# Kernel optimization log

Measured on AMD Instinct MI355X. Metric: run time of the kernel, lower is better.

Reference implementation:

```python
import jax, jax.numpy as jnp
import numpy as np

B, T, I, H = 64, 512, 1024, 1024


def setup_inputs() -> dict:
    key = jax.random.key(0)
    k1, k2, k3, k4 = jax.random.split(key, 4)
    scale_ih = (6.0 / (H + I)) ** 0.5  # xavier_uniform bound
    scale_hh = (6.0 / (H + H)) ** 0.5
    return {
        "x": jax.random.normal(k1, (B, T, I), dtype=jnp.float32),
        "h0": jax.random.normal(k2, (1, B, H), dtype=jnp.float32),
        "W_ih": jax.random.uniform(k3, (H, I), dtype=jnp.float32, minval=-scale_ih, maxval=scale_ih),
        "b_ih": jnp.zeros((H,), dtype=jnp.float32),
        "W_hh": jax.random.uniform(k4, (H, H), dtype=jnp.float32, minval=-scale_hh, maxval=scale_hh),
        "b_hh": jnp.zeros((H,), dtype=jnp.float32),
    }


def reference(x, h0, W_ih, b_ih, W_hh, b_hh):
    # h_t = tanh(x_t @ W_ih^T + b_ih + h_{t-1} @ W_hh^T + b_hh)
    # Precompute the input projection for all timesteps (same math, batched GEMM).
    xp = jnp.einsum("bti,hi->tbh", x, W_ih) + b_ih  # [T,B,H]
    h = h0[0]  # [B,H]

    def step(h, xp_t):
        h_new = jnp.tanh(xp_t + h @ W_hh.T + b_hh)
        return h_new, h_new

    _, ys = jax.lax.scan(step, h, xp)  # ys: [T,B,H]
    return jnp.transpose(ys, (1, 0, 2))  # [B,T,H]
```

## Files before the change

kernel.cpp:

```cpp
#include <hip/hip_runtime.h>
#include <hip/hip_bf16.h>

#define BB_   64
#define TT_   512
#define II_   1024
#define HH_   1024

typedef _Float16 half8  __attribute__((ext_vector_type(8)));
typedef _Float16 half4v __attribute__((ext_vector_type(4)));
typedef float    f32x4  __attribute__((ext_vector_type(4)));

__global__ __launch_bounds__(256) void gemm_xp(const float* __restrict__ x,
                                               const float* __restrict__ Wih,
                                               const float* __restrict__ bih,
                                               float* __restrict__ out) {
    __shared__ alignas(16) _Float16 As[128 * 40];
    __shared__ alignas(16) _Float16 Bs[128 * 40];

    const int tid  = threadIdx.x;
    const int bm   = blockIdx.x >> 3;
    const int bn   = blockIdx.x & 7;
    const int M0   = bm * 128, N0 = bn * 128;
    const int lane = tid & 63, w = tid >> 6;
    const int wm   = (w & 1) * 64, wn = (w >> 1) * 64;
    const int ro   = lane & 15, q = lane >> 4;
    const int sr   = tid >> 3, sc = tid & 7;

    const f32x4 zero4 = {0.f, 0.f, 0.f, 0.f};
    f32x4 acc[4][4];
    #pragma unroll
    for (int i = 0; i < 4; ++i)
        #pragma unroll
        for (int j = 0; j < 4; ++j) acc[i][j] = zero4;

    for (int kk = 0; kk < 32; ++kk) {
        const int k0 = kk * 32;
        #pragma unroll
        for (int ir = 0; ir < 4; ++ir) {
            const int row = ir * 32 + sr;
            const float4 av = *(const float4*)(x   + (size_t)(M0 + row) * II_ + k0 + sc * 4);
            const float4 bv = *(const float4*)(Wih + (size_t)(N0 + row) * II_ + k0 + sc * 4);
            half4v ah = { (_Float16)av.x, (_Float16)av.y, (_Float16)av.z, (_Float16)av.w };
            half4v bh = { (_Float16)bv.x, (_Float16)bv.y, (_Float16)bv.z, (_Float16)bv.w };
            *(half4v*)(As + row * 40 + sc * 4) = ah;
            *(half4v*)(Bs + row * 40 + sc * 4) = bh;
        }
        __syncthreads();

        half8 a[4], b[4];
        #pragma unroll
        for (int i = 0; i < 4; ++i) {
            a[i] = *(const half8*)(As + (wm + i * 16 + ro) * 40 + q * 8);
            b[i] = *(const half8*)(Bs + (wn + i * 16 + ro) * 40 + q * 8);
        }
        #pragma unroll
        for (int i = 0; i < 4; ++i)
            #pragma unroll
            for (int j = 0; j < 4; ++j)
                acc[i][j] = __builtin_amdgcn_mfma_f32_16x16x32_f16(a[i], b[j], acc[i][j], 0, 0, 0);
        __syncthreads();
    }

    #pragma unroll
    for (int j = 0; j < 4; ++j) {
        const int col = N0 + wn + j * 16 + ro;
        const float bias = bih[col];
        #pragma unroll
        for (int i = 0; i < 4; ++i) {
            #pragma unroll
            for (int r = 0; r < 4; ++r) {
                const int rowg = M0 + wm + i * 16 + q * 4 + r;
                out[(size_t)rowg * HH_ + col] = acc[i][j][r] + bias;
            }
        }
    }
}

__global__ __launch_bounds__(256, 1) void rnn_steps(const float* __restrict__ Whh,
                                                    const float* __restrict__ bhh,
                                                    const float* __restrict__ h0,
                                                    float* __restrict__ out,
                                                    unsigned* __restrict__ comm) {
    __shared__ alignas(16) _Float16 hbuf[2][5][1032];

    const int tid  = threadIdx.x;
    const int lane = tid & 63;
    const int w    = tid >> 6;
    const int g    = blockIdx.x >> 4;
    const int wg   = blockIdx.x & 15;
    const int b0   = g * 4;
    const int j0   = wg * 64;
    const int ro   = lane & 15, q = lane >> 4;
    const int arow  = (ro < 4) ? ro : 4;
    const int mycol = j0 + w * 16 + ro;

    half8 wf[4][8];
    {
        const float* wrow = Whh + (size_t)mycol * HH_;
        #pragma unroll
        for (int kq = 0; kq < 4; ++kq) {
            #pragma unroll
            for (int ks = 0; ks < 8; ++ks) {
                const int kc = kq * 256 + ks * 32 + q * 8;
                const float4 w0 = *(const float4*)(wrow + kc);
                const float4 w1 = *(const float4*)(wrow + kc + 4);
                half8 hv;
                hv[0] = (_Float16)w0.x; hv[1] = (_Float16)w0.y;
                hv[2] = (_Float16)w0.z; hv[3] = (_Float16)w0.w;
                hv[4] = (_Float16)w1.x; hv[5] = (_Float16)w1.y;
                hv[6] = (_Float16)w1.z; hv[7] = (_Float16)w1.w;
                wf[kq][ks] = hv;
            }
        }
    }
    const float bhh_r = bhh[mycol];

    for (int i = tid; i < 1032; i += 256) {
        hbuf[0][4][i] = (_Float16)0.f;
        hbuf[1][4][i] = (_Float16)0.f;
    }

    const f32x4 zero4 = {0.f, 0.f, 0.f, 0.f};

    for (int s = 0; s < TT_; ++s) {
        const int slot = s & 1;

        float xpv[4];
        if (q == 0) {
            #pragma unroll
            for (int r = 0; r < 4; ++r)
                xpv[r] = out[((size_t)(b0 + r) * TT_ + s) * HH_ + mycol];
        }

        _Float16* dst = &hbuf[slot][w][0];
        if (s == 0) {
            const float* hrow = h0 + (size_t)(b0 + w) * HH_;
            #pragma unroll
            for (int i = 0; i < 16; ++i)
                dst[i * 64 + lane] = (_Float16)hrow[i * 64 + lane];
        } else {
            unsigned* src = comm + (size_t)slot * (BB_ * HH_) + (size_t)(b0 + w) * HH_;
            unsigned v[16];
            #pragma unroll
            for (int i = 0; i < 16; ++i) v[i] = 0u;
            bool ok = false;
            while (!ok) {
                ok = true;
                #pragma unroll
                for (int i = 0; i < 16; ++i) {
                    if ((v[i] >> 16) != (unsigned)s) {
                        v[i] = __hip_atomic_load(src + i * 64 + lane,
                                                 __ATOMIC_RELAXED,
                                                 __HIP_MEMORY_SCOPE_AGENT);
                        ok = false;
                    }
                }
            }
            #pragma unroll
            for (int i = 0; i < 16; ++i) {
                union { unsigned short u; _Float16 h; } cv;
                cv.u = (unsigned short)(v[i] & 0xffffu);
                dst[i * 64 + lane] = cv.h;
            }
        }
        __syncthreads();

        f32x4 acc[4] = {zero4, zero4, zero4, zero4};
        const _Float16* abase = &hbuf[slot][0][0] + (size_t)arow * 1032;
        #pragma unroll
        for (int kq = 0; kq < 4; ++kq) {
            #pragma unroll
            for (int ks = 0; ks < 8; ++ks) {
                const half8 a = *(const half8*)(abase + kq * 256 + ks * 32 + q * 8);
                acc[kq] = __builtin_amdgcn_mfma_f32_16x16x32_f16(a, wf[kq][ks], acc[kq], 0, 0, 0);
            }
        }

        if (q == 0) {
            const unsigned tag = (unsigned)(s + 1) << 16;
            unsigned* cdst = comm + (size_t)((s + 1) & 1) * (BB_ * HH_);
            #pragma unroll
            for (int r = 0; r < 4; ++r) {
                const float pre  = xpv[r] + bhh_r
                                 + acc[0][r] + acc[1][r] + acc[2][r] + acc[3][r];
                const float hnew = tanhf(pre);
                out[((size_t)(b0 + r) * TT_ + s) * HH_ + mycol] = hnew;
                union { _Float16 h; unsigned short u; } cv; cv.h = (_Float16)hnew;
                __hip_atomic_store(cdst + (size_t)(b0 + r) * HH_ + mycol,
                                   tag | (unsigned)cv.u, __ATOMIC_RELAXED,
                                   __HIP_MEMORY_SCOPE_AGENT);
            }
        }
    }
}

extern "C" void kernel_launch(void* const* d_in, const int* in_sizes, int n_in,
                              void* d_out, int out_size, void* d_ws, size_t ws_size,
                              hipStream_t stream) {
    (void)in_sizes; (void)n_in; (void)out_size; (void)ws_size;

    const float* x   = (const float*)d_in[0];
    const float* h0  = (const float*)d_in[1];
    const float* Wih = (const float*)d_in[2];
    const float* bih = (const float*)d_in[3];
    const float* Whh = (const float*)d_in[4];
    const float* bhh = (const float*)d_in[5];
    float* out = (float*)d_out;

    unsigned* comm = (unsigned*)d_ws;

    gemm_xp<<<2048, 256, 0, stream>>>(x, Wih, bih, out);
    rnn_steps<<<256, 256, 0, stream>>>(Whh, bhh, h0, out, comm);
}
```

Baseline: 1.596 ms.

## Co-locate RNN batch groups per XCD and use cache-local polling for step handoff

Remaps block indices so each batch group's 16 workgroups land on the same XCD. At startup the blocks read HW_REG_XCC_ID to check that placement, and if it holds they poll neighbours' hidden states with sc0 dwordx2 loads, falling back to agent-scope atomics after a bounded spin count. The epilogue is spread across all four lane quads with shuffles, so every lane handles one batch row instead of only quad 0. tanhf is replaced by an exp2/rcp approximation. The aim is lower cross-XCD synchronization latency and a shorter serial per-step epilogue, at the cost of relying on the hardware's block-to-XCD dispatch pattern, on non-coherent cache behaviour, and on a less accurate tanh.

```diff
diff --git a/kernel.cpp b/kernel.cpp
--- a/kernel.cpp
+++ b/kernel.cpp
@@ -9,6 +9,12 @@
 typedef _Float16 half8  __attribute__((ext_vector_type(8)));
 typedef _Float16 half4v __attribute__((ext_vector_type(4)));
 typedef float    f32x4  __attribute__((ext_vector_type(4)));
+
+__device__ __forceinline__ float fast_tanh(float x) {
+    float t = fminf(fmaxf(x, -16.f), 16.f);
+    float e = __builtin_amdgcn_exp2f(t * 2.885390082f);
+    return 1.f - 2.f * __builtin_amdgcn_rcpf(e + 1.f);
+}
 
 __global__ __launch_bounds__(256) void gemm_xp(const float* __restrict__ x,
                                                const float* __restrict__ Wih,
@@ -86,17 +92,30 @@
     const int tid  = threadIdx.x;
     const int lane = tid & 63;
     const int w    = tid >> 6;
-    const int g    = blockIdx.x >> 4;
-    const int wg   = blockIdx.x & 15;
+    const int bidx = blockIdx.x;
+    const int cxcd = bidx & 7;
+    const int idx  = bidx >> 3;
+    const int g    = cxcd * 2 + (idx >> 4);
+    const int wg   = idx & 15;
     const int b0   = g * 4;
     const int j0   = wg * 64;
     const int ro   = lane & 15, q = lane >> 4;
-    const int arow  = (ro < 4) ? ro : 4;
-    const int mycol = j0 + w * 16 + ro;
+    const int arow = (ro < 4) ? ro : 4;
+    const int bat  = lane >> 4;
+    const int colw = j0 + w * 16 + (lane & 15);
+
+    unsigned* xsl = comm + (size_t)(4 * g) * HH_;
+
+    unsigned xcd;
+    asm volatile("s_getreg_b32 %0, hwreg(HW_REG_XCC_ID)" : "=s"(xcd));
+    xcd &= 15u;
+    if (tid == 0)
+        __hip_atomic_store(&xsl[wg], 0x5A5A0000u | xcd,
+                           __ATOMIC_RELAXED, __HIP_MEMORY_SCOPE_AGENT);
 
     half8 wf[4][8];
     {
-        const float* wrow = Whh + (size_t)mycol * HH_;
+        const float* wrow = Whh + (size_t)(j0 + w * 16 + ro) * HH_;
         #pragma unroll
         for (int kq = 0; kq < 4; ++kq) {
             #pragma unroll
@@ -113,55 +132,121 @@
             }
         }
     }
-    const float bhh_r = bhh[mycol];
+    const float bhh_r = bhh[colw];
 
     for (int i = tid; i < 1032; i += 256) {
         hbuf[0][4][i] = (_Float16)0.f;
         hbuf[1][4][i] = (_Float16)0.f;
     }
 
+    int fastw;
+    {
+        int allsame = 0;
+        for (;;) {
+            unsigned v[16]; int done = 1;
+            #pragma unroll
+            for (int i = 0; i < 16; ++i) {
+                v[i] = __hip_atomic_load(&xsl[i], __ATOMIC_RELAXED,
+                                         __HIP_MEMORY_SCOPE_AGENT);
+                done &= ((v[i] & 0xFFFF0000u) == 0x5A5A0000u);
+            }
+            if (done) {
+                allsame = 1;
+                #pragma unroll
+                for (int i = 0; i < 16; ++i) allsame &= (v[i] == v[0]);
+                break;
+            }
+            __builtin_amdgcn_s_sleep(8);
+        }
+        fastw = __builtin_amdgcn_readfirstlane(allsame);
+    }
+
     const f32x4 zero4 = {0.f, 0.f, 0.f, 0.f};
+
+    #define TAGOK_(v) ((((unsigned)((v) >> 16) & 0xffffu) == su) & \
+                       ((unsigned)((v) >> 48) == su))
 
     for (int s = 0; s < TT_; ++s) {
         const int slot = s & 1;
 
-        float xpv[4];
-        if (q == 0) {
-            #pragma unroll
-            for (int r = 0; r < 4; ++r)
-                xpv[r] = out[((size_t)(b0 + r) * TT_ + s) * HH_ + mycol];
-        }
-
-        _Float16* dst = &hbuf[slot][w][0];
+        const float xpv = out[((size_t)(b0 + bat) * TT_ + s) * HH_ + colw];
+
+        unsigned* dstw = (unsigned*)(&hbuf[slot][w][0]);
         if (s == 0) {
-            const float* hrow = h0 + (size_t)(b0 + w) * HH_;
-            #pragma unroll
-            for (int i = 0; i < 16; ++i)
-                dst[i * 64 + lane] = (_Float16)hrow[i * 64 + lane];
+            const float2* hrow = (const float2*)(h0 + (size_t)(b0 + w) * HH_);
+            #pragma unroll
+            for (int c = 0; c < 8; ++c) {
+                const float2 hv = hrow[c * 64 + lane];
+                union { _Float16 h[2]; unsigned u; } pk;
+                pk.h[0] = (_Float16)hv.x; pk.h[1] = (_Float16)hv.y;
+                dstw[c * 64 + lane] = pk.u;
+            }
         } else {
-            unsigned* src = comm + (size_t)slot * (BB_ * HH_) + (size_t)(b0 + w) * HH_;
-            unsigned v[16];
-            #pragma unroll
-            for (int i = 0; i < 16; ++i) v[i] = 0u;
+            const unsigned* srcw = comm + (size_t)slot * (BB_ * HH_)
+                                        + (size_t)(b0 + w) * HH_;
+            const unsigned su = (unsigned)s;
+            unsigned long long v0, v1, v2, v3, v4, v5, v6, v7;
             bool ok = false;
-            while (!ok) {
-                ok = true;
-                #pragma unroll
-                for (int i = 0; i < 16; ++i) {
-                    if ((v[i] >> 16) != (unsigned)s) {
-                        v[i] = __hip_atomic_load(src + i * 64 + lane,
-                                                 __ATOMIC_RELAXED,
-                                                 __HIP_MEMORY_SCOPE_AGENT);
-                        ok = false;
-                    }
+
+            if (fastw) {
+                const unsigned* p0 = srcw + 0 * 128 + 2 * lane;
+                const unsigned* p1 = srcw + 1 * 128 + 2 * lane;
+                const unsigned* p2 = srcw + 2 * 128 + 2 * lane;
+                const unsigned* p3 = srcw + 3 * 128 + 2 * lane;
+                const unsigned* p4 = srcw + 4 * 128 + 2 * lane;
+                const unsigned* p5 = srcw + 5 * 128 + 2 * lane;
+                const unsigned* p6 = srcw + 6 * 128 + 2 * lane;
+                const unsigned* p7 = srcw + 7 * 128 + 2 * lane;
+                int spins = 0;
+                while (!ok && spins < 32) {
+                    asm volatile("global_load_dwordx2 %0, %1, off sc0" : "=v"(v0) : "v"(p0));
+                    asm volatile("global_load_dwordx2 %0, %1, off sc0" : "=v"(v1) : "v"(p1));
+                    asm volatile("global_load_dwordx2 %0, %1, off sc0" : "=v"(v2) : "v"(p2));
+                    asm volatile("global_load_dwordx2 %0, %1, off sc0" : "=v"(v3) : "v"(p3));
+                    asm volatile("global_load_dwordx2 %0, %1, off sc0" : "=v"(v4) : "v"(p4));
+                    asm volatile("global_load_dwordx2 %0, %1, off sc0" : "=v"(v5) : "v"(p5));
+                    asm volatile("global_load_dwordx2 %0, %1, off sc0" : "=v"(v6) : "v"(p6));
+                    asm volatile("global_load_dwordx2 %0, %1, off sc0" : "=v"(v7) : "v"(p7));
+                    asm volatile("s_waitcnt vmcnt(0)"
+                                 : "+v"(v0), "+v"(v1), "+v"(v2), "+v"(v3),
+                                   "+v"(v4), "+v"(v5), "+v"(v6), "+v"(v7)
+                                 :: "memory");
+                    __builtin_amdgcn_sched_barrier(0);
+                    bool o = true;
+                    o &= TAGOK_(v0); o &= TAGOK_(v1); o &= TAGOK_(v2); o &= TAGOK_(v3);
+                    o &= TAGOK_(v4); o &= TAGOK_(v5); o &= TAGOK_(v6); o &= TAGOK_(v7);
+                    ok = o;
+                    ++spins;
                 }
-            }
-            #pragma unroll
-            for (int i = 0; i < 16; ++i) {
-                union { unsigned short u; _Float16 h; } cv;
-                cv.u = (unsigned short)(v[i] & 0xffffu);
-                dst[i * 64 + lane] = cv.h;
-            }
+                if (!__all(ok)) fastw = 0;
+            }
+            if (!ok) {
+                const unsigned long long* sp = (const unsigned long long*)srcw;
+                while (!ok) {
+                    v0 = __hip_atomic_load(sp + 0 * 64 + lane, __ATOMIC_RELAXED, __HIP_MEMORY_SCOPE_AGENT);
+                    v1 = __hip_atomic_load(sp + 1 * 64 + lane, __ATOMIC_RELAXED, __HIP_MEMORY_SCOPE_AGENT);
+                    v2 = __hip_atomic_load(sp + 2 * 64 + lane, __ATOMIC_RELAXED, __HIP_MEMORY_SCOPE_AGENT);
+                    v3 = __hip_atomic_load(sp + 3 * 64 + lane, __ATOMIC_RELAXED, __HIP_MEMORY_SCOPE_AGENT);
+                    v4 = __hip_atomic_load(sp + 4 * 64 + lane, __ATOMIC_RELAXED, __HIP_MEMORY_SCOPE_AGENT);
+                    v5 = __hip_atomic_load(sp + 5 * 64 + lane, __ATOMIC_RELAXED, __HIP_MEMORY_SCOPE_AGENT);
+                    v6 = __hip_atomic_load(sp + 6 * 64 + lane, __ATOMIC_RELAXED, __HIP_MEMORY_SCOPE_AGENT);
+                    v7 = __hip_atomic_load(sp + 7 * 64 + lane, __ATOMIC_RELAXED, __HIP_MEMORY_SCOPE_AGENT);
+                    bool o = true;
+                    o &= TAGOK_(v0); o &= TAGOK_(v1); o &= TAGOK_(v2); o &= TAGOK_(v3);
+                    o &= TAGOK_(v4); o &= TAGOK_(v5); o &= TAGOK_(v6); o &= TAGOK_(v7);
+                    ok = o;
+                }
+            }
+            #define PACK_(v) ((unsigned)((v) & 0xffffull) | (((unsigned)((v) >> 32)) << 16))
+            dstw[0 * 64 + lane] = PACK_(v0);
+            dstw[1 * 64 + lane] = PACK_(v1);
+            dstw[2 * 64 + lane] = PACK_(v2);
+            dstw[3 * 64 + lane] = PACK_(v3);
+            dstw[4 * 64 + lane] = PACK_(v4);
+            dstw[5 * 64 + lane] = PACK_(v5);
+            dstw[6 * 64 + lane] = PACK_(v6);
+            dstw[7 * 64 + lane] = PACK_(v7);
+            #undef PACK_
         }
         __syncthreads();
 
@@ -176,22 +261,24 @@
             }
         }
 
-        if (q == 0) {
-            const unsigned tag = (unsigned)(s + 1) << 16;
-            unsigned* cdst = comm + (size_t)((s + 1) & 1) * (BB_ * HH_);
-            #pragma unroll
-            for (int r = 0; r < 4; ++r) {
-                const float pre  = xpv[r] + bhh_r
-                                 + acc[0][r] + acc[1][r] + acc[2][r] + acc[3][r];
-                const float hnew = tanhf(pre);
-                out[((size_t)(b0 + r) * TT_ + s) * HH_ + mycol] = hnew;
-                union { _Float16 h; unsigned short u; } cv; cv.h = (_Float16)hnew;
-                __hip_atomic_store(cdst + (size_t)(b0 + r) * HH_ + mycol,
-                                   tag | (unsigned)cv.u, __ATOMIC_RELAXED,
-                                   __HIP_MEMORY_SCOPE_AGENT);
-            }
-        }
-    }
+        const f32x4 sum = acc[0] + acc[1] + acc[2] + acc[3];
+        const float t0 = __shfl(sum[0], lane & 15);
+        const float t1 = __shfl(sum[1], lane & 15);
+        const float t2 = __shfl(sum[2], lane & 15);
+        const float t3 = __shfl(sum[3], lane & 15);
+        const float val = (bat == 0) ? t0 : (bat == 1) ? t1 : (bat == 2) ? t2 : t3;
+
+        const float hnew = fast_tanh(xpv + bhh_r + val);
+
+        out[((size_t)(b0 + bat) * TT_ + s) * HH_ + colw] = hnew;
+
+        union { _Float16 h; unsigned short us; } cv; cv.h = (_Float16)hnew;
+        const unsigned word = ((unsigned)(s + 1) << 16) | (unsigned)cv.us;
+        unsigned* cdst = comm + (size_t)((s + 1) & 1) * (BB_ * HH_)
+                              + (size_t)(b0 + bat) * HH_ + colw;
+        __hip_atomic_store(cdst, word, __ATOMIC_RELAXED, __HIP_MEMORY_SCOPE_AGENT);
+    }
+    #undef TAGOK_
 }
 
 extern "C" void kernel_launch(void* const* d_in, const int* in_sizes, int n_in,
```

Result: slower. 1.632 ms (+2.3%).

## Regroup RNN recurrence into 32 blocks of 16 batch rows with wider polling

Applied to the files above, without the earlier changes.

Rebuilds the persistent recurrence kernel so each of 32 blocks of 512 threads handles 16 batch rows and 128 hidden columns, replacing 256 blocks that each handled 4 rows. All 16 MFMA rows are now useful instead of 4 plus padding, and polling of the tagged comm buffer uses 64-bit loads that fetch two tagged values at once. It also swaps tanhf for an exp2/rcp approximation and stores the comm value before writing the output. The cost is fewer CUs doing the per-step work, which lengthens each step's compute and reduces parallelism in exchange for fewer blocks taking part in the cross-block handshake.

```diff
diff --git a/kernel.cpp b/kernel.cpp
--- a/kernel.cpp
+++ b/kernel.cpp
@@ -9,6 +9,12 @@
 typedef _Float16 half8  __attribute__((ext_vector_type(8)));
 typedef _Float16 half4v __attribute__((ext_vector_type(4)));
 typedef float    f32x4  __attribute__((ext_vector_type(4)));
+
+__device__ __forceinline__ float fast_tanh(float x) {
+    float t = fminf(fmaxf(x, -16.f), 16.f);
+    float e = __builtin_amdgcn_exp2f(t * 2.885390082f);
+    return 1.f - 2.f * __builtin_amdgcn_rcpf(e + 1.f);
+}
 
 __global__ __launch_bounds__(256) void gemm_xp(const float* __restrict__ x,
                                                const float* __restrict__ Wih,
@@ -76,27 +82,26 @@
     }
 }
 
-__global__ __launch_bounds__(256, 1) void rnn_steps(const float* __restrict__ Whh,
+__global__ __launch_bounds__(512, 2) void rnn_steps(const float* __restrict__ Whh,
                                                     const float* __restrict__ bhh,
                                                     const float* __restrict__ h0,
                                                     float* __restrict__ out,
                                                     unsigned* __restrict__ comm) {
-    __shared__ alignas(16) _Float16 hbuf[2][5][1032];
+    __shared__ alignas(16) _Float16 hbuf[2][16][1032];
 
     const int tid  = threadIdx.x;
     const int lane = tid & 63;
     const int w    = tid >> 6;
-    const int g    = blockIdx.x >> 4;
-    const int wg   = blockIdx.x & 15;
-    const int b0   = g * 4;
-    const int j0   = wg * 64;
+    const int g    = blockIdx.x >> 3;
+    const int wg   = blockIdx.x & 7;
+    const int b0   = g * 16;
+    const int j0   = wg * 128;
     const int ro   = lane & 15, q = lane >> 4;
-    const int arow  = (ro < 4) ? ro : 4;
-    const int mycol = j0 + w * 16 + ro;
+    const int col  = j0 + w * 16 + ro;
 
     half8 wf[4][8];
     {
-        const float* wrow = Whh + (size_t)mycol * HH_;
+        const float* wrow = Whh + (size_t)col * HH_;
         #pragma unroll
         for (int kq = 0; kq < 4; ++kq) {
             #pragma unroll
@@ -113,60 +118,69 @@
             }
         }
     }
-    const float bhh_r = bhh[mycol];
-
-    for (int i = tid; i < 1032; i += 256) {
-        hbuf[0][4][i] = (_Float16)0.f;
-        hbuf[1][4][i] = (_Float16)0.f;
-    }
-
+    const float bhh_r = bhh[col];
     const f32x4 zero4 = {0.f, 0.f, 0.f, 0.f};
+
+    #define TAGOK_(v) ((((unsigned)((v) >> 16) & 0xffffu) == su) & \
+                       ((unsigned)((v) >> 48) == su))
 
     for (int s = 0; s < TT_; ++s) {
         const int slot = s & 1;
 
         float xpv[4];
-        if (q == 0) {
-            #pragma unroll
-            for (int r = 0; r < 4; ++r)
-                xpv[r] = out[((size_t)(b0 + r) * TT_ + s) * HH_ + mycol];
-        }
-
-        _Float16* dst = &hbuf[slot][w][0];
+        #pragma unroll
+        for (int r = 0; r < 4; ++r)
+            xpv[r] = out[((size_t)(b0 + q * 4 + r) * TT_ + s) * HH_ + col];
+
+        unsigned* dst0 = (unsigned*)(&hbuf[slot][2 * w][0]);
+        unsigned* dst1 = (unsigned*)(&hbuf[slot][2 * w + 1][0]);
         if (s == 0) {
-            const float* hrow = h0 + (size_t)(b0 + w) * HH_;
-            #pragma unroll
-            for (int i = 0; i < 16; ++i)
-                dst[i * 64 + lane] = (_Float16)hrow[i * 64 + lane];
+            #pragma unroll
+            for (int rr = 0; rr < 2; ++rr) {
+                const float2* hrow = (const float2*)(h0 + (size_t)(b0 + 2 * w + rr) * HH_);
+                unsigned* d = rr ? dst1 : dst0;
+                #pragma unroll
+                for (int c = 0; c < 8; ++c) {
+                    const float2 hv = hrow[c * 64 + lane];
+                    union { _Float16 h[2]; unsigned u; } pk;
+                    pk.h[0] = (_Float16)hv.x; pk.h[1] = (_Float16)hv.y;
+                    d[c * 64 + lane] = pk.u;
+                }
+            }
         } else {
-            unsigned* src = comm + (size_t)slot * (BB_ * HH_) + (size_t)(b0 + w) * HH_;
-            unsigned v[16];
-            #pragma unroll
-            for (int i = 0; i < 16; ++i) v[i] = 0u;
+            const unsigned su = (unsigned)s;
+            const unsigned long long* sp0 = (const unsigned long long*)
+                (comm + (size_t)slot * (BB_ * HH_) + (size_t)(b0 + 2 * w) * HH_);
+            const unsigned long long* sp1 = (const unsigned long long*)
+                (comm + (size_t)slot * (BB_ * HH_) + (size_t)(b0 + 2 * w + 1) * HH_);
+            unsigned long long v[16];
+            #pragma unroll
+            for (int i = 0; i < 16; ++i) v[i] = 0ull;
             bool ok = false;
             while (!ok) {
                 ok = true;
                 #pragma unroll
                 for (int i = 0; i < 16; ++i) {
-                    if ((v[i] >> 16) != (unsigned)s) {
-                        v[i] = __hip_atomic_load(src + i * 64 + lane,
+                    if (!TAGOK_(v[i])) {
+                        const unsigned long long* sp = (i < 8) ? sp0 : sp1;
+                        v[i] = __hip_atomic_load(sp + (i & 7) * 64 + lane,
                                                  __ATOMIC_RELAXED,
                                                  __HIP_MEMORY_SCOPE_AGENT);
                         ok = false;
                     }
                 }
             }
-            #pragma unroll
-            for (int i = 0; i < 16; ++i) {
-                union { unsigned short u; _Float16 h; } cv;
-                cv.u = (unsigned short)(v[i] & 0xffffu);
-                dst[i * 64 + lane] = cv.h;
-            }
+            #define PACK_(x) ((unsigned)((x) & 0xffffull) | (((unsigned)((x) >> 32)) << 16))
+            #pragma unroll
+            for (int i = 0; i < 8; ++i)  dst0[i * 64 + lane] = PACK_(v[i]);
+            #pragma unroll
+            for (int i = 8; i < 16; ++i) dst1[(i - 8) * 64 + lane] = PACK_(v[i]);
+            #undef PACK_
         }
         __syncthreads();
 
         f32x4 acc[4] = {zero4, zero4, zero4, zero4};
-        const _Float16* abase = &hbuf[slot][0][0] + (size_t)arow * 1032;
+        const _Float16* abase = &hbuf[slot][0][0] + (size_t)ro * 1032;
         #pragma unroll
         for (int kq = 0; kq < 4; ++kq) {
             #pragma unroll
@@ -176,22 +190,23 @@
             }
         }
 
-        if (q == 0) {
-            const unsigned tag = (unsigned)(s + 1) << 16;
-            unsigned* cdst = comm + (size_t)((s + 1) & 1) * (BB_ * HH_);
-            #pragma unroll
-            for (int r = 0; r < 4; ++r) {
-                const float pre  = xpv[r] + bhh_r
-                                 + acc[0][r] + acc[1][r] + acc[2][r] + acc[3][r];
-                const float hnew = tanhf(pre);
-                out[((size_t)(b0 + r) * TT_ + s) * HH_ + mycol] = hnew;
-                union { _Float16 h; unsigned short u; } cv; cv.h = (_Float16)hnew;
-                __hip_atomic_store(cdst + (size_t)(b0 + r) * HH_ + mycol,
-                                   tag | (unsigned)cv.u, __ATOMIC_RELAXED,
-                                   __HIP_MEMORY_SCOPE_AGENT);
-            }
-        }
-    }
+        const f32x4 sum = acc[0] + acc[1] + acc[2] + acc[3];
+        const unsigned tagn = (unsigned)(s + 1) << 16;
+        unsigned* cbase = comm + (size_t)((s + 1) & 1) * (BB_ * HH_);
+        float hn[4];
+        #pragma unroll
+        for (int r = 0; r < 4; ++r) {
+            hn[r] = fast_tanh(xpv[r] + bhh_r + sum[r]);
+            union { _Float16 h; unsigned short us; } cv; cv.h = (_Float16)hn[r];
+            __hip_atomic_store(cbase + (size_t)(b0 + q * 4 + r) * HH_ + col,
+                               tagn | (unsigned)cv.us, __ATOMIC_RELAXED,
+                               __HIP_MEMORY_SCOPE_AGENT);
+        }
+        #pragma unroll
+        for (int r = 0; r < 4; ++r)
+            out[((size_t)(b0 + q * 4 + r) * TT_ + s) * HH_ + col] = hn[r];
+    }
+    #undef TAGOK_
 }
 
 extern "C" void kernel_launch(void* const* d_in, const int* in_sizes, int n_in,
@@ -210,5 +225,5 @@
     unsigned* comm = (unsigned*)d_ws;
 
     gemm_xp<<<2048, 256, 0, stream>>>(x, Wih, bih, out);
-    rnn_steps<<<256, 256, 0, stream>>>(Whh, bhh, h0, out, comm);
-}
+    rnn_steps<<<32, 512, 0, stream>>>(Whh, bhh, h0, out, comm);
+}
```

Result: slower. 2.285 ms (+43.1%).
